# Kernel optimization log

Hardware: AMD Instinct MI355X
Metric: run time of the kernel (lower is better)

The kernel has to match this reference:

```python
import jax, jax.numpy as jnp
import numpy as np

LN_EPS = 1e-5


def setup_inputs() -> dict:
    key = jax.random.key(0)
    k1, k2, k3 = jax.random.split(key, 3)
    N, IN_DIM, D_MODEL, B = 1_000_000, 128, 128, 1024
    node_emb = jax.random.normal(k1, (N, IN_DIM), dtype=jnp.float32)
    batch_idx = jnp.sort(jax.random.randint(k2, (N,), 0, B, dtype=jnp.int32))
    # Linear params (kaiming-uniform-ish scale), LayerNorm affine params
    scale = 1.0 / np.sqrt(IN_DIM)
    W = jax.random.uniform(k3, (IN_DIM, D_MODEL), dtype=jnp.float32, minval=-scale, maxval=scale)
    b = jnp.zeros((D_MODEL,), dtype=jnp.float32)
    gamma = jnp.ones((D_MODEL,), dtype=jnp.float32)
    beta = jnp.zeros((D_MODEL,), dtype=jnp.float32)
    return {"node_emb": node_emb, "batch_idx": batch_idx, "batch_size": B,
            "W": W, "b": b, "gamma": gamma, "beta": beta}


def reference(node_emb, batch_idx, batch_size, W, b, gamma, beta):
    # Linear -> GELU (exact erf, torch default) -> Dropout (eval: identity) -> LayerNorm
    h = jax.nn.gelu(node_emb @ W + b, approximate=False)
    mu = jnp.mean(h, axis=-1, keepdims=True)
    var = jnp.mean((h - mu) ** 2, axis=-1, keepdims=True)
    node_proj = (h - mu) * jax.lax.rsqrt(var + LN_EPS) * gamma + beta  # [N, D]

    N = node_proj.shape[0]
    counts = jnp.bincount(batch_idx, length=batch_size)          # [B] nodes per graph
    starts = jnp.cumsum(counts) - counts                          # group start offsets
    pos = jnp.arange(N) - starts[batch_idx]                       # within-graph position
    T = int(jnp.max(counts))                                      # padded token length

    # Single scatter into padded [B, T, D] buffer (replaces split + pad_sequence)
    tokens = jnp.zeros((batch_size, T, node_proj.shape[1]), dtype=node_proj.dtype)
    tokens = tokens.at[batch_idx, pos].set(node_proj)
    enc_mask = (jnp.arange(T)[None, :] < counts[:, None]).astype(jnp.int32)  # [B, T]
    return tokens, enc_mask
```

## Files before the change

kernel.cpp:

```cpp
#include <hip/hip_runtime.h>


#define NDIM 128

typedef __attribute__((ext_vector_type(8))) short bf16x8;
typedef __attribute__((ext_vector_type(4))) float f32x4;

__device__ __forceinline__ short f2bf(float f) {
    unsigned u = __builtin_bit_cast(unsigned, f);
    unsigned r = (u + 0x7fffu + ((u >> 16) & 1u)) >> 16;
    return (short)r;
}

__global__ void starts_kernel(const int* __restrict__ bidx, int N, int B,
                              int* __restrict__ starts) {
    int b = blockIdx.x * blockDim.x + threadIdx.x;
    if (b > B) return;
    int lo = 0, hi = N;
    while (lo < hi) {
        int mid = (lo + hi) >> 1;
        if (bidx[mid] < b) lo = mid + 1; else hi = mid;
    }
    starts[b] = lo;
}

__global__ void pad_mask_kernel(const int* __restrict__ starts,
                                float* __restrict__ out, int T, int B) {
    const int b = blockIdx.y;
    const int idx = blockIdx.x * blockDim.x + threadIdx.x;
    const int t = idx >> 5;
    const int q = idx & 31;
    if (t >= T) return;
    const int cnt = starts[b + 1] - starts[b];
    const size_t row = (size_t)b * T + t;
    if (t >= cnt) {
        float4 z = make_float4(0.f, 0.f, 0.f, 0.f);
        *reinterpret_cast<float4*>(out + row * NDIM + q * 4) = z;
    }
    if (q == 0) {
        out[(size_t)B * T * NDIM + row] = (t < cnt) ? 1.0f : 0.0f;
    }
}

__global__ __launch_bounds__(512) void fused_kernel(
    const float* __restrict__ X, const int* __restrict__ bidx,
    const float* __restrict__ W, const float* __restrict__ bias,
    const float* __restrict__ gamma, const float* __restrict__ beta,
    const int* __restrict__ starts, float* __restrict__ tokens,
    int ntiles, int T) {
    __shared__ short wlds[16384];

    const int tid = threadIdx.x;
    const int lane = tid & 63;
    const int wave = tid >> 6;
    const int g = lane >> 4;
    const int m = lane & 15;

#pragma unroll
    for (int i = 0; i < 4; ++i) {
        int s = i * 512 + tid;
        int lane_s = s & 63;
        int fi = s >> 6;
        int gs = lane_s >> 4, ms = lane_s & 15;
        int nts = fi >> 2, kss = fi & 3;
        const float* wp = W + (size_t)(kss * 32 + gs * 8) * NDIM + nts * 16 + ms;
        bf16x8 f;
#pragma unroll
        for (int j = 0; j < 8; ++j) f[j] = f2bf(wp[(size_t)j * NDIM]);
        *reinterpret_cast<bf16x8*>(&wlds[s * 8]) = f;
    }

    float bv[8], gv[8], btv[8];
#pragma unroll
    for (int nt = 0; nt < 8; ++nt) {
        int c = nt * 16 + m;
        bv[nt] = bias[c];
        gv[nt] = gamma[c];
        btv[nt] = beta[c];
    }
    __syncthreads();

    const int stride = gridDim.x * 8;
    const int trips = (ntiles + stride - 1) / stride;
    for (int it = 0; it < trips; ++it) {
        __syncthreads();
        const int tile = (it * gridDim.x + blockIdx.x) * 8 + wave;
        if (tile >= ntiles) continue;

        const int myrow = tile * 16 + m;
        const float* xp = X + (size_t)myrow * NDIM + g * 8;

        bf16x8 a[4];
#pragma unroll
        for (int ks = 0; ks < 4; ++ks) {
            float4 lo = *reinterpret_cast<const float4*>(xp + ks * 32);
            float4 hi = *reinterpret_cast<const float4*>(xp + ks * 32 + 4);
            a[ks][0] = f2bf(lo.x); a[ks][1] = f2bf(lo.y);
            a[ks][2] = f2bf(lo.z); a[ks][3] = f2bf(lo.w);
            a[ks][4] = f2bf(hi.x); a[ks][5] = f2bf(hi.y);
            a[ks][6] = f2bf(hi.z); a[ks][7] = f2bf(hi.w);
        }

        f32x4 acc[8];
#pragma unroll
        for (int nt = 0; nt < 8; ++nt) acc[nt] = (f32x4){0.f, 0.f, 0.f, 0.f};
#pragma unroll
        for (int nt = 0; nt < 8; ++nt) {
#pragma unroll
            for (int ks = 0; ks < 4; ++ks) {
                bf16x8 bf = *reinterpret_cast<const bf16x8*>(
                    &wlds[((nt * 4 + ks) * 64 + lane) * 8]);
                acc[nt] = __builtin_amdgcn_mfma_f32_16x16x32_bf16(
                    a[ks], bf, acc[nt], 0, 0, 0);
            }
        }

#pragma unroll
        for (int nt = 0; nt < 8; ++nt) {
#pragma unroll
            for (int r = 0; r < 4; ++r) {
                float v = acc[nt][r] + bv[nt];
                float q = v * v;
                float t1 = fmaf(q, 0.044715f, 1.0f);
                float u = v * t1 * -1.5957691216f;
                float e = __expf(u);
                acc[nt][r] = __fdividef(v, 1.0f + e);
            }
        }

#pragma unroll
        for (int r = 0; r < 4; ++r) {
            float s = 0.f, sq = 0.f;
#pragma unroll
            for (int nt = 0; nt < 8; ++nt) {
                float v = acc[nt][r];
                s += v;
                sq += v * v;
            }
#pragma unroll
            for (int off = 1; off < 16; off <<= 1) {
                s += __shfl_xor(s, off, 64);
                sq += __shfl_xor(sq, off, 64);
            }
            float mu = s * (1.0f / 128.0f);
            float var = sq * (1.0f / 128.0f) - mu * mu;
            float rstd = rsqrtf(var + 1e-5f);
#pragma unroll
            for (int nt = 0; nt < 8; ++nt)
                acc[nt][r] = (acc[nt][r] - mu) * rstd * gv[nt] + btv[nt];
        }

        const int myb = bidx[myrow];
        const int myorow = myb * T + (myrow - starts[myb]);
#pragma unroll
        for (int r = 0; r < 4; ++r) {
            int orow = __shfl(myorow, g * 4 + r, 64);
            float* op = tokens + (size_t)orow * NDIM + m;
#pragma unroll
            for (int nt = 0; nt < 8; ++nt) op[nt * 16] = acc[nt][r];
        }
    }
}

extern "C" void kernel_launch(void* const* d_in, const int* in_sizes, int n_in,
                              void* d_out, int out_size, void* d_ws, size_t ws_size,
                              hipStream_t stream) {
    const float* X     = (const float*)d_in[0];
    const int*   bidx  = (const int*)d_in[1];
    const float* W     = (const float*)d_in[3];
    const float* bias  = (const float*)d_in[4];
    const float* gamma = (const float*)d_in[5];
    const float* beta  = (const float*)d_in[6];
    float* out = (float*)d_out;

    const int B = 1024;
    const int N = in_sizes[0] / NDIM;
    const int T = out_size / (B * (NDIM + 1));

    int* starts = (int*)d_ws;

    starts_kernel<<<dim3((B + 1 + 255) / 256), dim3(256), 0, stream>>>(bidx, N, B, starts);

    dim3 gridB((T * 32 + 255) / 256, B);
    pad_mask_kernel<<<gridB, dim3(256), 0, stream>>>(starts, out, T, B);

    const int ntiles = N / 16;
    const int nblocks = 1568;
    fused_kernel<<<dim3(nblocks), dim3(512), 0, stream>>>(
        X, bidx, W, bias, gamma, beta, starts, out, ntiles, T);
}
```

Baseline: 278.9 us.

## Software-pipeline X loads with double buffering in persistent per-wave fused kernel

The fused kernel becomes a persistent per-wave loop that prefetches the next tile's X rows into registers while computing the current tile, and drops the per-iteration block barrier. Block size shrinks to 256 threads with an occupancy hint and the grid shrinks to 768 blocks. The pad/mask kernel is reorganized to one block per graph that writes only the padding region and mask. bf16 conversion uses the library intrinsic. The double buffers raise register pressure, which could lower occupancy.

```diff
diff --git a/kernel.cpp b/kernel.cpp
--- a/kernel.cpp
+++ b/kernel.cpp
@@ -1,4 +1,5 @@
 #include <hip/hip_runtime.h>
+#include <hip/hip_bf16.h>
 
 
 #define NDIM 128
@@ -7,9 +8,7 @@
 typedef __attribute__((ext_vector_type(4))) float f32x4;
 
 __device__ __forceinline__ short f2bf(float f) {
-    unsigned u = __builtin_bit_cast(unsigned, f);
-    unsigned r = (u + 0x7fffu + ((u >> 16) & 1u)) >> 16;
-    return (short)r;
+    return __builtin_bit_cast(short, __float2bfloat16(f));
 }
 
 __global__ void starts_kernel(const int* __restrict__ bidx, int N, int B,
@@ -24,25 +23,98 @@
     starts[b] = lo;
 }
 
-__global__ void pad_mask_kernel(const int* __restrict__ starts,
-                                float* __restrict__ out, int T, int B) {
-    const int b = blockIdx.y;
-    const int idx = blockIdx.x * blockDim.x + threadIdx.x;
-    const int t = idx >> 5;
-    const int q = idx & 31;
-    if (t >= T) return;
+__global__ __launch_bounds__(256) void pad_mask_kernel(
+    const int* __restrict__ starts, float* __restrict__ out, int T, int B) {
+    const int b = blockIdx.x;
     const int cnt = starts[b + 1] - starts[b];
-    const size_t row = (size_t)b * T + t;
-    if (t >= cnt) {
-        float4 z = make_float4(0.f, 0.f, 0.f, 0.f);
-        *reinterpret_cast<float4*>(out + row * NDIM + q * 4) = z;
-    }
-    if (q == 0) {
-        out[(size_t)B * T * NDIM + row] = (t < cnt) ? 1.0f : 0.0f;
-    }
+    float* mask = out + (size_t)B * T * NDIM + (size_t)b * T;
+    for (int t = threadIdx.x; t < T; t += blockDim.x)
+        mask[t] = (t < cnt) ? 1.0f : 0.0f;
+    float4* pad = reinterpret_cast<float4*>(out + ((size_t)b * T + cnt) * NDIM);
+    const int n4 = (T - cnt) * (NDIM / 4);
+    float4 z = make_float4(0.f, 0.f, 0.f, 0.f);
+    for (int i = threadIdx.x; i < n4; i += blockDim.x) pad[i] = z;
 }
 
-__global__ __launch_bounds__(512) void fused_kernel(
+
+#define LOADX(BUF, TT)                                                        \
+    do {                                                                      \
+        int tc_ = (TT);                                                       \
+        if (tc_ >= ntiles) tc_ = ntiles - 1;                                  \
+        const float* xp_ = X + (size_t)(tc_ * 16 + m) * NDIM + g * 8;         \
+        BUF[0] = *reinterpret_cast<const f32x4*>(xp_);                        \
+        BUF[1] = *reinterpret_cast<const f32x4*>(xp_ + 4);                    \
+        BUF[2] = *reinterpret_cast<const f32x4*>(xp_ + 32);                   \
+        BUF[3] = *reinterpret_cast<const f32x4*>(xp_ + 36);                   \
+        BUF[4] = *reinterpret_cast<const f32x4*>(xp_ + 64);                   \
+        BUF[5] = *reinterpret_cast<const f32x4*>(xp_ + 68);                   \
+        BUF[6] = *reinterpret_cast<const f32x4*>(xp_ + 96);                   \
+        BUF[7] = *reinterpret_cast<const f32x4*>(xp_ + 100);                  \
+    } while (0)
+
+#define PROCESS(BUF, OBUF, TCUR, TPF)                                         \
+    do {                                                                      \
+        const int tcur_ = (TCUR);                                             \
+        LOADX(OBUF, (TPF));                                                   \
+        asm volatile("" ::: "memory");          \
+        f32x4 acc[8];                                                         \
+        _Pragma("unroll") for (int nt = 0; nt < 8; ++nt)                      \
+            acc[nt] = (f32x4){0.f, 0.f, 0.f, 0.f};                            \
+        _Pragma("unroll") for (int ks = 0; ks < 4; ++ks) {                    \
+            bf16x8 aks;                                                       \
+            _Pragma("unroll") for (int j = 0; j < 4; ++j) {                   \
+                aks[j] = f2bf(BUF[2 * ks][j]);                                \
+                aks[4 + j] = f2bf(BUF[2 * ks + 1][j]);                        \
+            }                                                                 \
+            _Pragma("unroll") for (int nt = 0; nt < 8; ++nt) {                \
+                bf16x8 bf = *reinterpret_cast<const bf16x8*>(                 \
+                    &wlds[((nt * 4 + ks) * 64 + lane) * 8]);                  \
+                acc[nt] = __builtin_amdgcn_mfma_f32_16x16x32_bf16(            \
+                    aks, bf, acc[nt], 0, 0, 0);                               \
+            }                                                                 \
+        }                                                                     \
+                                                        \
+        _Pragma("unroll") for (int nt = 0; nt < 8; ++nt) {                    \
+            _Pragma("unroll") for (int r = 0; r < 4; ++r) {                   \
+                float v = acc[nt][r] + bv[nt];                                \
+                float q = v * v;                                              \
+                float t1 = fmaf(q, 0.044715f, 1.0f);                          \
+                float u = v * t1 * -1.5957691216f;                            \
+                float e = __expf(u);                                          \
+                acc[nt][r] = __fdividef(v, 1.0f + e);                         \
+            }                                                                 \
+        }                                                                     \
+                                        \
+        _Pragma("unroll") for (int r = 0; r < 4; ++r) {                       \
+            float s = 0.f, sq = 0.f;                                          \
+            _Pragma("unroll") for (int nt = 0; nt < 8; ++nt) {                \
+                float v = acc[nt][r];                                         \
+                s += v;                                                       \
+                sq += v * v;                                                  \
+            }                                                                 \
+            _Pragma("unroll") for (int off = 1; off < 16; off <<= 1) {        \
+                s += __shfl_xor(s, off, 64);                                  \
+                sq += __shfl_xor(sq, off, 64);                                \
+            }                                                                 \
+            float mu = s * (1.0f / 128.0f);                                   \
+            float var = sq * (1.0f / 128.0f) - mu * mu;                       \
+            float rstd = rsqrtf(var + 1e-5f);                                 \
+            _Pragma("unroll") for (int nt = 0; nt < 8; ++nt)                  \
+                acc[nt][r] = (acc[nt][r] - mu) * rstd * gv[nt] + btv[nt];     \
+        }                                                                     \
+                                                  \
+        const int myrow_ = tcur_ * 16 + m;                                    \
+        const int myb_ = bidx[myrow_];                                        \
+        const int myorow_ = myb_ * T + (myrow_ - starts[myb_]);               \
+        _Pragma("unroll") for (int r = 0; r < 4; ++r) {                       \
+            int orow = __shfl(myorow_, g * 4 + r, 64);                        \
+            float* op = tokens + (size_t)orow * NDIM + m;                     \
+            _Pragma("unroll") for (int nt = 0; nt < 8; ++nt)                  \
+                op[nt * 16] = acc[nt][r];                                     \
+        }                                                                     \
+    } while (0)
+
+__global__ __launch_bounds__(256, 3) void fused_kernel(
     const float* __restrict__ X, const int* __restrict__ bidx,
     const float* __restrict__ W, const float* __restrict__ bias,
     const float* __restrict__ gamma, const float* __restrict__ beta,
@@ -57,8 +129,8 @@
     const int m = lane & 15;
 
 #pragma unroll
-    for (int i = 0; i < 4; ++i) {
-        int s = i * 512 + tid;
+    for (int i = 0; i < 8; ++i) {
+        int s = i * 256 + tid;
         int lane_s = s & 63;
         int fi = s >> 6;
         int gs = lane_s >> 4, ms = lane_s & 15;
@@ -80,85 +152,19 @@
     }
     __syncthreads();
 
-    const int stride = gridDim.x * 8;
-    const int trips = (ntiles + stride - 1) / stride;
-    for (int it = 0; it < trips; ++it) {
-        __syncthreads();
-        const int tile = (it * gridDim.x + blockIdx.x) * 8 + wave;
-        if (tile >= ntiles) continue;
+    const int nwaves = gridDim.x * 4;
+    const int wave_gid = blockIdx.x * 4 + wave;
 
-        const int myrow = tile * 16 + m;
-        const float* xp = X + (size_t)myrow * NDIM + g * 8;
-
-        bf16x8 a[4];
-#pragma unroll
-        for (int ks = 0; ks < 4; ++ks) {
-            float4 lo = *reinterpret_cast<const float4*>(xp + ks * 32);
-            float4 hi = *reinterpret_cast<const float4*>(xp + ks * 32 + 4);
-            a[ks][0] = f2bf(lo.x); a[ks][1] = f2bf(lo.y);
-            a[ks][2] = f2bf(lo.z); a[ks][3] = f2bf(lo.w);
-            a[ks][4] = f2bf(hi.x); a[ks][5] = f2bf(hi.y);
-            a[ks][6] = f2bf(hi.z); a[ks][7] = f2bf(hi.w);
-        }
-
-        f32x4 acc[8];
-#pragma unroll
-        for (int nt = 0; nt < 8; ++nt) acc[nt] = (f32x4){0.f, 0.f, 0.f, 0.f};
-#pragma unroll
-        for (int nt = 0; nt < 8; ++nt) {
-#pragma unroll
-            for (int ks = 0; ks < 4; ++ks) {
-                bf16x8 bf = *reinterpret_cast<const bf16x8*>(
-                    &wlds[((nt * 4 + ks) * 64 + lane) * 8]);
-                acc[nt] = __builtin_amdgcn_mfma_f32_16x16x32_bf16(
-                    a[ks], bf, acc[nt], 0, 0, 0);
-            }
-        }
-
-#pragma unroll
-        for (int nt = 0; nt < 8; ++nt) {
-#pragma unroll
-            for (int r = 0; r < 4; ++r) {
-                float v = acc[nt][r] + bv[nt];
-                float q = v * v;
-                float t1 = fmaf(q, 0.044715f, 1.0f);
-                float u = v * t1 * -1.5957691216f;
-                float e = __expf(u);
-                acc[nt][r] = __fdividef(v, 1.0f + e);
-            }
-        }
-
-#pragma unroll
-        for (int r = 0; r < 4; ++r) {
-            float s = 0.f, sq = 0.f;
-#pragma unroll
-            for (int nt = 0; nt < 8; ++nt) {
-                float v = acc[nt][r];
-                s += v;
-                sq += v * v;
-            }
-#pragma unroll
-            for (int off = 1; off < 16; off <<= 1) {
-                s += __shfl_xor(s, off, 64);
-                sq += __shfl_xor(sq, off, 64);
-            }
-            float mu = s * (1.0f / 128.0f);
-            float var = sq * (1.0f / 128.0f) - mu * mu;
-            float rstd = rsqrtf(var + 1e-5f);
-#pragma unroll
-            for (int nt = 0; nt < 8; ++nt)
-                acc[nt][r] = (acc[nt][r] - mu) * rstd * gv[nt] + btv[nt];
-        }
-
-        const int myb = bidx[myrow];
-        const int myorow = myb * T + (myrow - starts[myb]);
-#pragma unroll
-        for (int r = 0; r < 4; ++r) {
-            int orow = __shfl(myorow, g * 4 + r, 64);
-            float* op = tokens + (size_t)orow * NDIM + m;
-#pragma unroll
-            for (int nt = 0; nt < 8; ++nt) op[nt * 16] = acc[nt][r];
-        }
+    f32x4 bufA[8], bufB[8];
+    int t = wave_gid;
+    LOADX(bufA, t);
+    while (true) {
+        PROCESS(bufA, bufB, t, t + nwaves);
+        t += nwaves;
+        if (t >= ntiles) break;
+        PROCESS(bufB, bufA, t, t + nwaves);
+        t += nwaves;
+        if (t >= ntiles) break;
     }
 }
 
@@ -181,11 +187,10 @@
 
     starts_kernel<<<dim3((B + 1 + 255) / 256), dim3(256), 0, stream>>>(bidx, N, B, starts);
 
-    dim3 gridB((T * 32 + 255) / 256, B);
-    pad_mask_kernel<<<gridB, dim3(256), 0, stream>>>(starts, out, T, B);
+    pad_mask_kernel<<<dim3(B), dim3(256), 0, stream>>>(starts, out, T, B);
 
     const int ntiles = N / 16;
-    const int nblocks = 1568;
-    fused_kernel<<<dim3(nblocks), dim3(512), 0, stream>>>(
+    const int nblocks = 768;
+    fused_kernel<<<dim3(nblocks), dim3(256), 0, stream>>>(
         X, bidx, W, bias, gamma, beta, starts, out, ntiles, T);
 }
```

Measured after the change: 243.3 us. 1.15x faster.

## Software-pipeline X loads across persistent wave tiles and simplify padding kernel

Applied to the files above, without the earlier changes.

The fused kernel becomes a persistent per-wave loop that prefetches the next tile's fp32 rows into registers while the current tile runs MFMA, GELU, LayerNorm and the scatter store. Blocks shrink to 256 threads with a 4-blocks-per-CU launch bound, and the grid drops to 1024 blocks. The padding kernel now runs one block per graph, zeroing only that graph's padded rows and writing its mask row, instead of launching a thread per padded position. bf16 conversion switches to the library intrinsic. The extra prefetch registers add pressure and could lower occupancy.

```diff
diff --git a/kernel.cpp b/kernel.cpp
--- a/kernel.cpp
+++ b/kernel.cpp
@@ -1,4 +1,5 @@
 #include <hip/hip_runtime.h>
+#include <hip/hip_bf16.h>
 
 
 #define NDIM 128
@@ -7,9 +8,7 @@
 typedef __attribute__((ext_vector_type(4))) float f32x4;
 
 __device__ __forceinline__ short f2bf(float f) {
-    unsigned u = __builtin_bit_cast(unsigned, f);
-    unsigned r = (u + 0x7fffu + ((u >> 16) & 1u)) >> 16;
-    return (short)r;
+    return __builtin_bit_cast(short, __float2bfloat16(f));
 }
 
 __global__ void starts_kernel(const int* __restrict__ bidx, int N, int B,
@@ -24,25 +23,46 @@
     starts[b] = lo;
 }
 
-__global__ void pad_mask_kernel(const int* __restrict__ starts,
-                                float* __restrict__ out, int T, int B) {
-    const int b = blockIdx.y;
-    const int idx = blockIdx.x * blockDim.x + threadIdx.x;
-    const int t = idx >> 5;
-    const int q = idx & 31;
-    if (t >= T) return;
+__global__ __launch_bounds__(256) void pad_mask_kernel(
+    const int* __restrict__ starts, float* __restrict__ out, int T, int B) {
+    const int b = blockIdx.x;
     const int cnt = starts[b + 1] - starts[b];
-    const size_t row = (size_t)b * T + t;
-    if (t >= cnt) {
-        float4 z = make_float4(0.f, 0.f, 0.f, 0.f);
-        *reinterpret_cast<float4*>(out + row * NDIM + q * 4) = z;
-    }
-    if (q == 0) {
-        out[(size_t)B * T * NDIM + row] = (t < cnt) ? 1.0f : 0.0f;
-    }
-}
-
-__global__ __launch_bounds__(512) void fused_kernel(
+    float* mask = out + (size_t)B * T * NDIM + (size_t)b * T;
+    for (int t = threadIdx.x; t < T; t += blockDim.x)
+        mask[t] = (t < cnt) ? 1.0f : 0.0f;
+    float4* pad = reinterpret_cast<float4*>(out + ((size_t)b * T + cnt) * NDIM);
+    const int n4 = (T - cnt) * (NDIM / 4);
+    float4 z = make_float4(0.f, 0.f, 0.f, 0.f);
+    for (int i = threadIdx.x; i < n4; i += blockDim.x) pad[i] = z;
+}
+
+
+#define LOADX(RAW, TT)                                                        \
+    do {                                                                      \
+        int tc_ = (TT);                                                       \
+        if (tc_ >= ntiles) tc_ = ntiles - 1;                                  \
+        const float* xp_ = X + (size_t)(tc_ * 16 + m) * NDIM + g * 8;         \
+        RAW[0] = *reinterpret_cast<const f32x4*>(xp_);                        \
+        RAW[1] = *reinterpret_cast<const f32x4*>(xp_ + 4);                    \
+        RAW[2] = *reinterpret_cast<const f32x4*>(xp_ + 32);                   \
+        RAW[3] = *reinterpret_cast<const f32x4*>(xp_ + 36);                   \
+        RAW[4] = *reinterpret_cast<const f32x4*>(xp_ + 64);                   \
+        RAW[5] = *reinterpret_cast<const f32x4*>(xp_ + 68);                   \
+        RAW[6] = *reinterpret_cast<const f32x4*>(xp_ + 96);                   \
+        RAW[7] = *reinterpret_cast<const f32x4*>(xp_ + 100);                  \
+    } while (0)
+
+#define CONVERT(RAW, AB)                                                      \
+    do {                                                                      \
+        _Pragma("unroll") for (int ks = 0; ks < 4; ++ks) {                    \
+            _Pragma("unroll") for (int j = 0; j < 4; ++j) {                   \
+                AB[ks][j] = f2bf(RAW[2 * ks][j]);                             \
+                AB[ks][4 + j] = f2bf(RAW[2 * ks + 1][j]);                     \
+            }                                                                 \
+        }                                                                     \
+    } while (0)
+
+__global__ __launch_bounds__(256, 4) void fused_kernel(
     const float* __restrict__ X, const int* __restrict__ bidx,
     const float* __restrict__ W, const float* __restrict__ bias,
     const float* __restrict__ gamma, const float* __restrict__ beta,
@@ -57,8 +77,8 @@
     const int m = lane & 15;
 
 #pragma unroll
-    for (int i = 0; i < 4; ++i) {
-        int s = i * 512 + tid;
+    for (int i = 0; i < 8; ++i) {
+        int s = i * 256 + tid;
         int lane_s = s & 63;
         int fi = s >> 6;
         int gs = lane_s >> 4, ms = lane_s & 15;
@@ -80,40 +100,36 @@
     }
     __syncthreads();
 
-    const int stride = gridDim.x * 8;
-    const int trips = (ntiles + stride - 1) / stride;
-    for (int it = 0; it < trips; ++it) {
-        __syncthreads();
-        const int tile = (it * gridDim.x + blockIdx.x) * 8 + wave;
-        if (tile >= ntiles) continue;
-
-        const int myrow = tile * 16 + m;
-        const float* xp = X + (size_t)myrow * NDIM + g * 8;
-
-        bf16x8 a[4];
+    const int nw = gridDim.x * 4;
+    const int wave_gid = blockIdx.x * 4 + wave;
+
+    f32x4 raw[8];
+    bf16x8 abuf[4];
+    int t = wave_gid;
+    LOADX(raw, t);
+    CONVERT(raw, abuf);
+
+    while (true) {
+        LOADX(raw, t + nw);
+        asm volatile("" ::: "memory");
+
+        f32x4 acc[8];
+#pragma unroll
+        for (int nt = 0; nt < 8; ++nt) acc[nt] = (f32x4){0.f, 0.f, 0.f, 0.f};
 #pragma unroll
         for (int ks = 0; ks < 4; ++ks) {
-            float4 lo = *reinterpret_cast<const float4*>(xp + ks * 32);
-            float4 hi = *reinterpret_cast<const float4*>(xp + ks * 32 + 4);
-            a[ks][0] = f2bf(lo.x); a[ks][1] = f2bf(lo.y);
-            a[ks][2] = f2bf(lo.z); a[ks][3] = f2bf(lo.w);
-            a[ks][4] = f2bf(hi.x); a[ks][5] = f2bf(hi.y);
-            a[ks][6] = f2bf(hi.z); a[ks][7] = f2bf(hi.w);
-        }
-
-        f32x4 acc[8];
-#pragma unroll
-        for (int nt = 0; nt < 8; ++nt) acc[nt] = (f32x4){0.f, 0.f, 0.f, 0.f};
-#pragma unroll
-        for (int nt = 0; nt < 8; ++nt) {
-#pragma unroll
-            for (int ks = 0; ks < 4; ++ks) {
+#pragma unroll
+            for (int nt = 0; nt < 8; ++nt) {
                 bf16x8 bf = *reinterpret_cast<const bf16x8*>(
                     &wlds[((nt * 4 + ks) * 64 + lane) * 8]);
                 acc[nt] = __builtin_amdgcn_mfma_f32_16x16x32_bf16(
-                    a[ks], bf, acc[nt], 0, 0, 0);
-            }
-        }
+                    abuf[ks], bf, acc[nt], 0, 0, 0);
+            }
+        }
+
+        const int myrow = t * 16 + m;
+        const int myb = bidx[myrow];
+        const int myorow = myb * T + (myrow - starts[myb]);
 
 #pragma unroll
         for (int nt = 0; nt < 8; ++nt) {
@@ -150,8 +166,6 @@
                 acc[nt][r] = (acc[nt][r] - mu) * rstd * gv[nt] + btv[nt];
         }
 
-        const int myb = bidx[myrow];
-        const int myorow = myb * T + (myrow - starts[myb]);
 #pragma unroll
         for (int r = 0; r < 4; ++r) {
             int orow = __shfl(myorow, g * 4 + r, 64);
@@ -159,6 +173,10 @@
 #pragma unroll
             for (int nt = 0; nt < 8; ++nt) op[nt * 16] = acc[nt][r];
         }
+
+        t += nw;
+        if (t >= ntiles) break;
+        CONVERT(raw, abuf);
     }
 }
 
@@ -181,11 +199,10 @@
 
     starts_kernel<<<dim3((B + 1 + 255) / 256), dim3(256), 0, stream>>>(bidx, N, B, starts);
 
-    dim3 gridB((T * 32 + 255) / 256, B);
-    pad_mask_kernel<<<gridB, dim3(256), 0, stream>>>(starts, out, T, B);
+    pad_mask_kernel<<<dim3(B), dim3(256), 0, stream>>>(starts, out, T, B);
 
     const int ntiles = N / 16;
-    const int nblocks = 1568;
-    fused_kernel<<<dim3(nblocks), dim3(512), 0, stream>>>(
+    const int nblocks = 1024;
+    fused_kernel<<<dim3(nblocks), dim3(256), 0, stream>>>(
         X, bidx, W, bias, gamma, beta, starts, out, ntiles, T);
 }
```

Result: faster. 240.8 us (-13.7%).
